# Kernel tuning notes

Measured on AMD Instinct MI355X. Metric: run time of the kernel, lower is better.

Reference implementation:

```python
import jax, jax.numpy as jnp
import numpy as np

B, N, G = 4096, 20, 4
D_IN, D_OUT, H = 128, 64, 8
LRELU = 0.2  # TF leaky_relu default alpha


def _glorot(key, shape):
    fan_in, fan_out = shape[-2], shape[-1]
    scale = jnp.sqrt(6.0 / (fan_in + fan_out)).astype(jnp.float32)
    return jax.random.uniform(key, shape, jnp.float32, -1.0, 1.0) * scale


def setup_inputs() -> dict:
    key = jax.random.key(0)
    k1, k2, k3, k4, k5, k6 = jax.random.split(key, 6)
    return {
        "self_vecs": jax.random.normal(k1, (B, G, D_IN), jnp.float32),
        "neigh_vecs": jax.random.normal(k2, (B, N, G, D_IN), jnp.float32),
        "W_heads": _glorot(k3, (H, D_IN, D_OUT)),      # per-head before_attend_weights
        "a_self": _glorot(k4, (H, D_OUT, 1))[..., 0],  # per-head attend_weights_self  [H, D_OUT]
        "a_neigh": _glorot(k5, (H, D_OUT, 1))[..., 0], # per-head attend_weights_neigh [H, D_OUT]
        "W_out": _glorot(k6, (H * D_OUT, D_OUT)),      # final FC weights
    }


def reference(self_vecs, neigh_vecs, W_heads, a_self, a_neigh, W_out):
    # Transform self and neighbor vectors for all heads at once.
    self_t = jnp.einsum("bgd,hde->bghe", self_vecs, W_heads)    # [B,G,H,E]
    neigh_t = jnp.einsum("bngd,hde->bnghe", neigh_vecs, W_heads)  # [B,N,G,H,E]

    f_self = jnp.einsum("bghe,he->bgh", self_t, a_self)          # [B,G,H]
    f_neigh = jnp.einsum("bnghe,he->bngh", neigh_t, a_neigh)     # [B,N,G,H]

    # logits [B,N,G,H]; original applies softmax over the num_graphs axis (tf default last axis of [B,N,G])
    logits = f_self[:, None, :, :] + f_neigh
    attend = jax.nn.softmax(jax.nn.leaky_relu(logits, LRELU), axis=2)  # softmax over G

    # Weighted aggregation over neighbors: [B,G,H,E]
    out_h = jnp.einsum("bngh,bnghe->bghe", attend, neigh_t)
    out_h = jax.nn.leaky_relu(out_h, LRELU)  # per-head activation (act=leaky_relu)

    # Concatenate heads along feature dim -> [B,G,H*E], final FC + relu
    h = out_h.reshape(out_h.shape[0], out_h.shape[1], H * D_OUT)
    return jax.nn.relu(jnp.einsum("bgk,ke->bge", h, W_out))
```

## Files before the change

kernel.cpp:

```cpp
#include <hip/hip_runtime.h>
#include <hip/hip_bf16.h>

#define BB 4096
#define NNB 20
#define GG 4
#define DIN 128
#define EE 64
#define HH 8

typedef short bf16x8 __attribute__((ext_vector_type(8)));
typedef float f32x4 __attribute__((ext_vector_type(4)));

__device__ __forceinline__ float lrelu_f(float x) { return x > 0.f ? x : 0.2f * x; }
__device__ __forceinline__ unsigned short f2bf(float f) {
  unsigned u = __float_as_uint(f);
  return (unsigned short)((u + 0x7fffu + ((u >> 16) & 1u)) >> 16);
}
__device__ __forceinline__ float bf2f(unsigned short s) {
  return __uint_as_float(((unsigned)s) << 16);
}

__global__ __launch_bounds__(256) void prep_kernel(
    const float* __restrict__ W_heads, const float* __restrict__ a_self,
    const float* __restrict__ a_neigh, const float* __restrict__ W_out,
    unsigned short* __restrict__ P1Whi, unsigned short* __restrict__ P1Wlo,
    unsigned short* __restrict__ WBhi, unsigned short* __restrict__ WBlo,
    unsigned short* __restrict__ WOhi, unsigned short* __restrict__ WOlo) {
  int id = blockIdx.x * 256 + threadIdx.x;
  if (id < 2048) {
    int j = id & 7, lane = (id >> 3) & 63, kb = id >> 9;
    int col = lane & 15, k = kb * 32 + (lane >> 4) * 8 + j;
    int h = col & 7;
    const float* a = (col < 8) ? a_neigh : a_self;
    const float* Wrow = W_heads + (h * DIN + k) * EE;
    float acc = 0.f;
    for (int e = 0; e < EE; ++e) acc = fmaf(Wrow[e], a[h * EE + e], acc);
    unsigned short hi = f2bf(acc);
    P1Whi[id] = hi;
    P1Wlo[id] = f2bf(acc - bf2f(hi));
  } else if (id < 2048 + 65536) {
    int rel = id - 2048;
    int j = rel & 7, l = (rel >> 3) & 63, kb = (rel >> 9) & 3, nt = (rel >> 11) & 3, h = rel >> 13;
    int d = kb * 32 + (l >> 4) * 8 + j;
    int e = nt * 16 + (l & 15);
    float w = W_heads[(h * DIN + d) * EE + e];
    unsigned short hi = f2bf(w);
    WBhi[rel] = hi;
    WBlo[rel] = f2bf(w - bf2f(hi));
  } else if (id < 2048 + 65536 + 32768) {
    int rel = id - 2048 - 65536;
    int j = rel & 7, l = (rel >> 3) & 63, kb = (rel >> 9) & 15, nt = rel >> 13;
    int k = kb * 32 + (l >> 4) * 8 + j;
    int n = nt * 16 + (l & 15);
    float w = W_out[k * EE + n];
    unsigned short hi = f2bf(w);
    WOhi[rel] = hi;
    WOlo[rel] = f2bf(w - bf2f(hi));
  }
}

__global__ __launch_bounds__(256) void fused_kernel(
    const float* __restrict__ self_vecs, const float* __restrict__ neigh_vecs,
    const unsigned short* __restrict__ P1Whi, const unsigned short* __restrict__ P1Wlo,
    const unsigned short* __restrict__ WBhi, const unsigned short* __restrict__ WBlo,
    const unsigned short* __restrict__ WOhi, const unsigned short* __restrict__ WOlo,
    float* __restrict__ out) {
  __shared__ char smem[65536];
  char* aggb = smem;
  float* f_s   = (float*)(smem + 32768);
  float* att_s = (float*)(smem + 32768 + 21504);
  char* hb = smem + 32768;

  const int t = threadIdx.x;
  const int w = t >> 6, lane = t & 63;
  const int m = lane & 15, kg = lane >> 4;
  const int bid = blockIdx.x;

  bf16x8 wfh[4], wfl[4];
#pragma unroll
  for (int kb = 0; kb < 4; ++kb) {
    wfh[kb] = *(const bf16x8*)(P1Whi + (kb * 64 + lane) * 8);
    wfl[kb] = *(const bf16x8*)(P1Wlo + (kb * 64 + lane) * 8);
  }

  const int bl_m = m >> 2, g_m = m & 3;
  for (int tile = w; tile < 21; tile += 4) {
    const float* rowp;
    if (tile < 20)
      rowp = neigh_vecs + (((size_t)(bid * 4 + bl_m) * NNB + tile) * GG + g_m) * DIN;
    else
      rowp = self_vecs + ((size_t)bid * 16 + m) * DIN;
    f32x4 c = {0.f, 0.f, 0.f, 0.f};
#pragma unroll
    for (int kb = 0; kb < 4; ++kb) {
      float4 xa = *(const float4*)(rowp + kb * 32 + kg * 8);
      float4 xb = *(const float4*)(rowp + kb * 32 + kg * 8 + 4);
      float xv[8] = {xa.x, xa.y, xa.z, xa.w, xb.x, xb.y, xb.z, xb.w};
      bf16x8 xh, xl;
#pragma unroll
      for (int j = 0; j < 8; ++j) {
        unsigned short hi = f2bf(xv[j]);
        xh[j] = (short)hi;
        xl[j] = (short)f2bf(xv[j] - bf2f(hi));
      }
      c = __builtin_amdgcn_mfma_f32_16x16x32_bf16(xh, wfh[kb], c, 0, 0, 0);
      c = __builtin_amdgcn_mfma_f32_16x16x32_bf16(xh, wfl[kb], c, 0, 0, 0);
      c = __builtin_amdgcn_mfma_f32_16x16x32_bf16(xl, wfh[kb], c, 0, 0, 0);
    }
#pragma unroll
    for (int reg = 0; reg < 4; ++reg)
      f_s[tile * 256 + (kg * 4 + reg) * 16 + m] = c[reg];
  }
  __syncthreads();

#pragma unroll
  for (int it = 0; it < 3; ++it) {
    int task = t + it * 256;
    if (task < 640) {
      int bl = task & 3, nh = task >> 2, n = nh >> 3, h = nh & 7;
      float l[4], mx = -1e30f;
#pragma unroll
      for (int gg = 0; gg < 4; ++gg) {
        int bg = bl * 4 + gg;
        float v = lrelu_f(f_s[20 * 256 + bg * 16 + 8 + h] + f_s[n * 256 + bg * 16 + h]);
        l[gg] = v;
        mx = fmaxf(mx, v);
      }
      float s = 0.f;
#pragma unroll
      for (int gg = 0; gg < 4; ++gg) { l[gg] = __expf(l[gg] - mx); s += l[gg]; }
      float inv = 1.f / s;
#pragma unroll
      for (int gg = 0; gg < 4; ++gg) att_s[n * 128 + (bl * 4 + gg) * 8 + h] = l[gg] * inv;
    }
  }
  __syncthreads();

  {
    const float* nbw = neigh_vecs + (size_t)(bid * 4 + w) * (NNB * GG * DIN);
#pragma unroll
    for (int g = 0; g < 4; ++g) {
      const int bg = w * 4 + g;
      float acc[8][2];
#pragma unroll
      for (int h = 0; h < 8; ++h) { acc[h][0] = 0.f; acc[h][1] = 0.f; }
      for (int n = 0; n < NNB; ++n) {
        float2 x2 = *(const float2*)&nbw[(n * GG + g) * DIN + 2 * lane];
        f32x4 a0 = *(const f32x4*)&att_s[n * 128 + bg * 8];
        f32x4 a1 = *(const f32x4*)&att_s[n * 128 + bg * 8 + 4];
#pragma unroll
        for (int h = 0; h < 4; ++h) {
          acc[h][0] = fmaf(a0[h], x2.x, acc[h][0]);
          acc[h][1] = fmaf(a0[h], x2.y, acc[h][1]);
          acc[h + 4][0] = fmaf(a1[h], x2.x, acc[h + 4][0]);
          acc[h + 4][1] = fmaf(a1[h], x2.y, acc[h + 4][1]);
        }
      }
      const int swz = (bg & 7) << 4;
#pragma unroll
      for (int h = 0; h < 8; ++h) {
        unsigned pack = (unsigned)f2bf(acc[h][0]) | ((unsigned)f2bf(acc[h][1]) << 16);
        *(unsigned*)(aggb + ((bg * 2048 + h * 256 + 4 * lane) ^ swz)) = pack;
      }
    }
  }
  __syncthreads();

  {
    const int aswz = (m & 7) << 4;
#pragma unroll
    for (int hi_ = 0; hi_ < 2; ++hi_) {
      const int hh = 2 * w + hi_;
      bf16x8 a[4];
#pragma unroll
      for (int kb = 0; kb < 4; ++kb)
        a[kb] = *(const bf16x8*)(aggb + ((m * 2048 + hh * 256 + kb * 64 + kg * 16) ^ aswz));
#pragma unroll
      for (int nt = 0; nt < 4; ++nt) {
        f32x4 c = {0.f, 0.f, 0.f, 0.f};
#pragma unroll
        for (int kb = 0; kb < 4; ++kb) {
          const int fi = (((hh * 4 + nt) * 4 + kb) * 64 + lane) * 8;
          bf16x8 bh = *(const bf16x8*)(WBhi + fi);
          bf16x8 bl_ = *(const bf16x8*)(WBlo + fi);
          c = __builtin_amdgcn_mfma_f32_16x16x32_bf16(a[kb], bh, c, 0, 0, 0);
          c = __builtin_amdgcn_mfma_f32_16x16x32_bf16(a[kb], bl_, c, 0, 0, 0);
        }
        const int k = hh * 64 + nt * 16 + m;
#pragma unroll
        for (int reg = 0; reg < 4; ++reg) {
          int lr = kg * 4 + reg;
          int byte = (lr * 2048 + k * 4) ^ ((lr & 7) << 4);
          *(float*)(hb + byte) = lrelu_f(c[reg]);
        }
      }
    }
  }
  __syncthreads();

  {
    const int swz = (m & 7) << 4;
    f32x4 acc = {0.f, 0.f, 0.f, 0.f};
    for (int kb = 0; kb < 16; ++kb) {
      const int base = m * 2048 + (kb * 32 + kg * 8) * 4;
      float4 f0 = *(const float4*)(hb + ((base)      ^ swz));
      float4 f1 = *(const float4*)(hb + ((base + 16) ^ swz));
      float fv[8] = {f0.x, f0.y, f0.z, f0.w, f1.x, f1.y, f1.z, f1.w};
      bf16x8 ahi, alo;
#pragma unroll
      for (int j = 0; j < 8; ++j) {
        unsigned short hi = f2bf(fv[j]);
        ahi[j] = (short)hi;
        alo[j] = (short)f2bf(fv[j] - bf2f(hi));
      }
      const int fi = ((w * 16 + kb) * 64 + lane) * 8;
      bf16x8 bh = *(const bf16x8*)(WOhi + fi);
      bf16x8 bl_ = *(const bf16x8*)(WOlo + fi);
      acc = __builtin_amdgcn_mfma_f32_16x16x32_bf16(ahi, bh, acc, 0, 0, 0);
      acc = __builtin_amdgcn_mfma_f32_16x16x32_bf16(ahi, bl_, acc, 0, 0, 0);
      acc = __builtin_amdgcn_mfma_f32_16x16x32_bf16(alo, bh, acc, 0, 0, 0);
    }
    const int rbase = bid * 16;
#pragma unroll
    for (int reg = 0; reg < 4; ++reg) {
      int row = rbase + kg * 4 + reg;
      out[(size_t)row * EE + w * 16 + m] = fmaxf(acc[reg], 0.f);
    }
  }
}

extern "C" void kernel_launch(void* const* d_in, const int* in_sizes, int n_in,
                              void* d_out, int out_size, void* d_ws, size_t ws_size,
                              hipStream_t stream) {
  (void)in_sizes; (void)n_in; (void)out_size; (void)ws_size;
  const float* self_vecs  = (const float*)d_in[0];
  const float* neigh_vecs = (const float*)d_in[1];
  const float* W_heads    = (const float*)d_in[2];
  const float* a_self     = (const float*)d_in[3];
  const float* a_neigh    = (const float*)d_in[4];
  const float* W_out      = (const float*)d_in[5];
  float* out              = (float*)d_out;

  char* ws = (char*)d_ws;
  unsigned short* P1Whi = (unsigned short*)ws;
  unsigned short* P1Wlo = (unsigned short*)(ws + 4096);
  unsigned short* WBhi  = (unsigned short*)(ws + 8192);
  unsigned short* WBlo  = (unsigned short*)(ws + 8192 + 131072);
  unsigned short* WOhi  = (unsigned short*)(ws + 8192 + 262144);
  unsigned short* WOlo  = (unsigned short*)(ws + 8192 + 262144 + 65536);

  prep_kernel<<<(2048 + 65536 + 32768) / 256, 256, 0, stream>>>(
      W_heads, a_self, a_neigh, W_out, P1Whi, P1Wlo, WBhi, WBlo, WOhi, WOlo);

  fused_kernel<<<BB / 4, 256, 0, stream>>>(
      self_vecs, neigh_vecs, P1Whi, P1Wlo, WBhi, WBlo, WOhi, WOlo, out);
}
```

Before: 76.55 us.

## Use 512-thread blocks, compact attention LDS, and store hidden activations as bf16

Doubles the block to 8 waves and redistributes every stage across them: tiles, softmax tasks, per-(b,g) aggregation rows, and one head per wave in the head GEMM. Only the needed halves of the logit projections are stored, in a smaller swizzled LDS layout, which cuts shared memory to about 53 KB. The hidden layer is written to LDS as a single bf16 value instead of fp32 and then split into hi/lo parts, so the final GEMM does two MFMAs per step instead of three. The cost is lower precision in the final FC and only half the waves being active in the last stage.

Result: faster. 67.86 us (-11.4%).

```diff
diff --git a/kernel.cpp b/kernel.cpp
--- a/kernel.cpp
+++ b/kernel.cpp
@@ -59,16 +59,16 @@
   }
 }
 
-__global__ __launch_bounds__(256) void fused_kernel(
+__global__ __launch_bounds__(512, 4) void fused_kernel(
     const float* __restrict__ self_vecs, const float* __restrict__ neigh_vecs,
     const unsigned short* __restrict__ P1Whi, const unsigned short* __restrict__ P1Wlo,
     const unsigned short* __restrict__ WBhi, const unsigned short* __restrict__ WBlo,
     const unsigned short* __restrict__ WOhi, const unsigned short* __restrict__ WOlo,
     float* __restrict__ out) {
-  __shared__ char smem[65536];
+  __shared__ char smem[53760];
   char* aggb = smem;
-  float* f_s   = (float*)(smem + 32768);
-  float* att_s = (float*)(smem + 32768 + 21504);
+  float* fw   = (float*)(smem + 32768);
+  float* attw = (float*)(smem + 43520);
   char* hb = smem + 32768;
 
   const int t = threadIdx.x;
@@ -84,7 +84,7 @@
   }
 
   const int bl_m = m >> 2, g_m = m & 3;
-  for (int tile = w; tile < 21; tile += 4) {
+  for (int tile = w; tile < 21; tile += 8) {
     const float* rowp;
     if (tile < 20)
       rowp = neigh_vecs + (((size_t)(bid * 4 + bl_m) * NNB + tile) * GG + g_m) * DIN;
@@ -107,22 +107,38 @@
       c = __builtin_amdgcn_mfma_f32_16x16x32_bf16(xh, wfl[kb], c, 0, 0, 0);
       c = __builtin_amdgcn_mfma_f32_16x16x32_bf16(xl, wfh[kb], c, 0, 0, 0);
     }
-#pragma unroll
-    for (int reg = 0; reg < 4; ++reg)
-      f_s[tile * 256 + (kg * 4 + reg) * 16 + m] = c[reg];
-  }
-  __syncthreads();
-
-#pragma unroll
-  for (int it = 0; it < 3; ++it) {
-    int task = t + it * 256;
+    if (tile < 20) {
+      if (m < 8) {
+#pragma unroll
+        for (int reg = 0; reg < 4; ++reg) {
+          int row = kg * 4 + reg;
+          fw[tile * 128 + ((row * 8 + m) ^ (kg << 3))] = c[reg];
+        }
+      }
+    } else {
+      if (m >= 8) {
+#pragma unroll
+        for (int reg = 0; reg < 4; ++reg) {
+          int row = kg * 4 + reg;
+          fw[20 * 128 + ((row * 8 + (m - 8)) ^ (kg << 3))] = c[reg];
+        }
+      }
+    }
+  }
+  __syncthreads();
+
+#pragma unroll
+  for (int it = 0; it < 2; ++it) {
+    int task = t + it * 512;
     if (task < 640) {
-      int bl = task & 3, nh = task >> 2, n = nh >> 3, h = nh & 7;
+      int bl = task & 3, h = (task >> 2) & 7, n = task >> 5;
       float l[4], mx = -1e30f;
 #pragma unroll
       for (int gg = 0; gg < 4; ++gg) {
         int bg = bl * 4 + gg;
-        float v = lrelu_f(f_s[20 * 256 + bg * 16 + 8 + h] + f_s[n * 256 + bg * 16 + h]);
+        float fn = fw[n * 128 + ((bg * 8 + h) ^ (bl << 3))];
+        float fs = fw[20 * 128 + ((bg * 8 + h) ^ (bl << 3))];
+        float v = lrelu_f(fs + fn);
         l[gg] = v;
         mx = fmaxf(mx, v);
       }
@@ -131,100 +147,88 @@
       for (int gg = 0; gg < 4; ++gg) { l[gg] = __expf(l[gg] - mx); s += l[gg]; }
       float inv = 1.f / s;
 #pragma unroll
-      for (int gg = 0; gg < 4; ++gg) att_s[n * 128 + (bl * 4 + gg) * 8 + h] = l[gg] * inv;
+      for (int gg = 0; gg < 4; ++gg)
+        attw[n * 128 + (((bl * 4 + gg) * 8 + h) ^ (bl << 3))] = l[gg] * inv;
+    }
+  }
+  __syncthreads();
+
+#pragma unroll
+  for (int i = 0; i < 2; ++i) {
+    const int bg = 2 * w + i;
+    const int bl = bg >> 2, g = bg & 3;
+    const float* nbw = neigh_vecs + ((size_t)(bid * 4 + bl) * NNB * GG + g) * DIN;
+    float acc[8][2];
+#pragma unroll
+    for (int h = 0; h < 8; ++h) { acc[h][0] = 0.f; acc[h][1] = 0.f; }
+    for (int n = 0; n < NNB; ++n) {
+      float2 x2 = *(const float2*)&nbw[(size_t)n * GG * DIN + 2 * lane];
+      const int abase = n * 128 + ((bg * 8) ^ (bl << 3));
+      f32x4 a0 = *(const f32x4*)&attw[abase];
+      f32x4 a1 = *(const f32x4*)&attw[abase + 4];
+#pragma unroll
+      for (int h = 0; h < 4; ++h) {
+        acc[h][0] = fmaf(a0[h], x2.x, acc[h][0]);
+        acc[h][1] = fmaf(a0[h], x2.y, acc[h][1]);
+        acc[h + 4][0] = fmaf(a1[h], x2.x, acc[h + 4][0]);
+        acc[h + 4][1] = fmaf(a1[h], x2.y, acc[h + 4][1]);
+      }
+    }
+    const int swz = (bg & 7) << 4;
+#pragma unroll
+    for (int h = 0; h < 8; ++h) {
+      unsigned pack = (unsigned)f2bf(acc[h][0]) | ((unsigned)f2bf(acc[h][1]) << 16);
+      *(unsigned*)(aggb + ((bg * 2048 + h * 256 + 4 * lane) ^ swz)) = pack;
     }
   }
   __syncthreads();
 
   {
-    const float* nbw = neigh_vecs + (size_t)(bid * 4 + w) * (NNB * GG * DIN);
-#pragma unroll
-    for (int g = 0; g < 4; ++g) {
-      const int bg = w * 4 + g;
-      float acc[8][2];
-#pragma unroll
-      for (int h = 0; h < 8; ++h) { acc[h][0] = 0.f; acc[h][1] = 0.f; }
-      for (int n = 0; n < NNB; ++n) {
-        float2 x2 = *(const float2*)&nbw[(n * GG + g) * DIN + 2 * lane];
-        f32x4 a0 = *(const f32x4*)&att_s[n * 128 + bg * 8];
-        f32x4 a1 = *(const f32x4*)&att_s[n * 128 + bg * 8 + 4];
-#pragma unroll
-        for (int h = 0; h < 4; ++h) {
-          acc[h][0] = fmaf(a0[h], x2.x, acc[h][0]);
-          acc[h][1] = fmaf(a0[h], x2.y, acc[h][1]);
-          acc[h + 4][0] = fmaf(a1[h], x2.x, acc[h + 4][0]);
-          acc[h + 4][1] = fmaf(a1[h], x2.y, acc[h + 4][1]);
-        }
-      }
-      const int swz = (bg & 7) << 4;
-#pragma unroll
-      for (int h = 0; h < 8; ++h) {
-        unsigned pack = (unsigned)f2bf(acc[h][0]) | ((unsigned)f2bf(acc[h][1]) << 16);
-        *(unsigned*)(aggb + ((bg * 2048 + h * 256 + 4 * lane) ^ swz)) = pack;
-      }
-    }
-  }
-  __syncthreads();
-
-  {
+    const int hh = w;
     const int aswz = (m & 7) << 4;
-#pragma unroll
-    for (int hi_ = 0; hi_ < 2; ++hi_) {
-      const int hh = 2 * w + hi_;
-      bf16x8 a[4];
-#pragma unroll
-      for (int kb = 0; kb < 4; ++kb)
-        a[kb] = *(const bf16x8*)(aggb + ((m * 2048 + hh * 256 + kb * 64 + kg * 16) ^ aswz));
-#pragma unroll
-      for (int nt = 0; nt < 4; ++nt) {
-        f32x4 c = {0.f, 0.f, 0.f, 0.f};
-#pragma unroll
-        for (int kb = 0; kb < 4; ++kb) {
-          const int fi = (((hh * 4 + nt) * 4 + kb) * 64 + lane) * 8;
-          bf16x8 bh = *(const bf16x8*)(WBhi + fi);
-          bf16x8 bl_ = *(const bf16x8*)(WBlo + fi);
-          c = __builtin_amdgcn_mfma_f32_16x16x32_bf16(a[kb], bh, c, 0, 0, 0);
-          c = __builtin_amdgcn_mfma_f32_16x16x32_bf16(a[kb], bl_, c, 0, 0, 0);
-        }
-        const int k = hh * 64 + nt * 16 + m;
-#pragma unroll
-        for (int reg = 0; reg < 4; ++reg) {
-          int lr = kg * 4 + reg;
-          int byte = (lr * 2048 + k * 4) ^ ((lr & 7) << 4);
-          *(float*)(hb + byte) = lrelu_f(c[reg]);
-        }
-      }
-    }
-  }
-  __syncthreads();
-
-  {
-    const int swz = (m & 7) << 4;
+    bf16x8 a[4];
+#pragma unroll
+    for (int kb = 0; kb < 4; ++kb)
+      a[kb] = *(const bf16x8*)(aggb + ((m * 2048 + hh * 256 + kb * 64 + kg * 16) ^ aswz));
+#pragma unroll
+    for (int nt = 0; nt < 4; ++nt) {
+      f32x4 c = {0.f, 0.f, 0.f, 0.f};
+#pragma unroll
+      for (int kb = 0; kb < 4; ++kb) {
+        const int fi = (((hh * 4 + nt) * 4 + kb) * 64 + lane) * 8;
+        bf16x8 bh = *(const bf16x8*)(WBhi + fi);
+        bf16x8 bl_ = *(const bf16x8*)(WBlo + fi);
+        c = __builtin_amdgcn_mfma_f32_16x16x32_bf16(a[kb], bh, c, 0, 0, 0);
+        c = __builtin_amdgcn_mfma_f32_16x16x32_bf16(a[kb], bl_, c, 0, 0, 0);
+      }
+      const int k = hh * 64 + nt * 16 + m;
+#pragma unroll
+      for (int reg = 0; reg < 4; ++reg) {
+        int row = kg * 4 + reg;
+        int byte = (row * 1024 + k * 2) ^ ((row & 7) << 4);
+        *(unsigned short*)(hb + byte) = f2bf(lrelu_f(c[reg]));
+      }
+    }
+  }
+  __syncthreads();
+
+  if (w < 4) {
+    const int nt = w;
     f32x4 acc = {0.f, 0.f, 0.f, 0.f};
     for (int kb = 0; kb < 16; ++kb) {
-      const int base = m * 2048 + (kb * 32 + kg * 8) * 4;
-      float4 f0 = *(const float4*)(hb + ((base)      ^ swz));
-      float4 f1 = *(const float4*)(hb + ((base + 16) ^ swz));
-      float fv[8] = {f0.x, f0.y, f0.z, f0.w, f1.x, f1.y, f1.z, f1.w};
-      bf16x8 ahi, alo;
-#pragma unroll
-      for (int j = 0; j < 8; ++j) {
-        unsigned short hi = f2bf(fv[j]);
-        ahi[j] = (short)hi;
-        alo[j] = (short)f2bf(fv[j] - bf2f(hi));
-      }
-      const int fi = ((w * 16 + kb) * 64 + lane) * 8;
+      int byte = (m * 1024 + (kb * 32 + kg * 8) * 2) ^ ((m & 7) << 4);
+      bf16x8 ah = *(const bf16x8*)(hb + byte);
+      const int fi = ((nt * 16 + kb) * 64 + lane) * 8;
       bf16x8 bh = *(const bf16x8*)(WOhi + fi);
       bf16x8 bl_ = *(const bf16x8*)(WOlo + fi);
-      acc = __builtin_amdgcn_mfma_f32_16x16x32_bf16(ahi, bh, acc, 0, 0, 0);
-      acc = __builtin_amdgcn_mfma_f32_16x16x32_bf16(ahi, bl_, acc, 0, 0, 0);
-      acc = __builtin_amdgcn_mfma_f32_16x16x32_bf16(alo, bh, acc, 0, 0, 0);
+      acc = __builtin_amdgcn_mfma_f32_16x16x32_bf16(ah, bh, acc, 0, 0, 0);
+      acc = __builtin_amdgcn_mfma_f32_16x16x32_bf16(ah, bl_, acc, 0, 0, 0);
     }
     const int rbase = bid * 16;
 #pragma unroll
     for (int reg = 0; reg < 4; ++reg) {
       int row = rbase + kg * 4 + reg;
-      out[(size_t)row * EE + w * 16 + m] = fmaxf(acc[reg], 0.f);
+      out[(size_t)row * EE + nt * 16 + m] = fmaxf(acc[reg], 0.f);
     }
   }
 }
@@ -252,6 +256,6 @@
   prep_kernel<<<(2048 + 65536 + 32768) / 256, 256, 0, stream>>>(
       W_heads, a_self, a_neigh, W_out, P1Whi, P1Wlo, WBhi, WBlo, WOhi, WOlo);
 
-  fused_kernel<<<BB / 4, 256, 0, stream>>>(
+  fused_kernel<<<BB / 4, 512, 0, stream>>>(
       self_vecs, neigh_vecs, P1Whi, P1Wlo, WBhi, WBlo, WOhi, WOlo, out);
 }
```
